# Performance work log

Hardware: AMD Instinct MI355X
Metric: run time of the kernel (lower is better)

## Reference

```python
import jax, jax.numpy as jnp
import numpy as np

N = 262144   # query points
M = 4096     # boundary points
D = 128      # d_model (m)
H = 4        # num_heads
HD = D // H  # head_dim = 32
L = 3        # num_layers
PI = float(np.pi)


def multi_feature_encoding(x):
    # x: [T, 2] -> [T, 30]; 15 fixed feature maps, hstacked
    feats = [
        x,
        x ** 2,
        (x - 1.5) ** 2,
        (x - 4.5) ** 2,
        jax.nn.sigmoid(x),
        jax.nn.sigmoid(x - 1.5),
        jax.nn.sigmoid(x - 4.5),
        x - 1.5,
        x - 4.5,
        jnp.sin(PI * x),
        jnp.cos(PI * x),
        jnp.sin(PI * x * 0.25),
        jnp.cos(PI * x * 0.25),
        jnp.sin(PI * x * 0.5),
        jnp.cos(PI * x * 0.5),
    ]
    return jnp.concatenate(feats, axis=-1)


def pos_encode(x, w, b):
    # w: [30, D], b: [D]
    return jnp.sin(multi_feature_encoding(x) @ w + b)


def setup_inputs() -> dict:
    key = jax.random.key(0)
    ks = jax.random.split(key, 24)
    s = 0.05

    def p(k, shape):
        return jax.random.normal(k, shape, dtype=jnp.float32) * s

    return {
        "query_pts": jax.random.normal(ks[0], (N, 2), dtype=jnp.float32),
        "boundary_pts": jax.random.normal(ks[1], (M, 2), dtype=jnp.float32),
        # positional encoders (query / boundary)
        "pe_w": p(ks[2], (30, D)), "pe_b": p(ks[3], (D,)),
        "bpe_w": p(ks[4], (30, D)), "bpe_b": p(ks[5], (D,)),
        # per-layer per-head q/k/v projections, stacked: [L, H, D, HD]
        "Wq": p(ks[6], (L, H, D, HD)), "bq": p(ks[7], (L, H, HD)),
        "Wk": p(ks[8], (L, H, D, HD)), "bk": p(ks[9], (L, H, HD)),
        "Wv": p(ks[10], (L, H, D, HD)), "bv": p(ks[11], (L, H, HD)),
        # attention out proj and FFN (two D->D linears) per layer
        "Wo": p(ks[12], (L, D, D)), "bo": p(ks[13], (L, D)),
        "W1": p(ks[14], (L, D, D)), "b1": p(ks[15], (L, D)),
        "W2": p(ks[16], (L, D, D)), "b2": p(ks[17], (L, D)),
        # final projector: D -> D//2 -> 3
        "pw1": p(ks[18], (D, D // 2)), "pb1": p(ks[19], (D // 2,)),
        "pw2": p(ks[20], (D // 2, 3)), "pb2": p(ks[21], (3,)),
    }


def reference(query_pts, boundary_pts, pe_w, pe_b, bpe_w, bpe_b,
              Wq, bq, Wk, bk, Wv, bv, Wo, bo, W1, b1, W2, b2,
              pw1, pb1, pw2, pb2):
    h = pos_encode(query_pts, pe_w, pe_b)[None]        # [1, N, D]
    b_enc = pos_encode(boundary_pts, bpe_w, bpe_b)[None]  # [1, M, D]

    for l in range(L):
        # batched per-head projections (equivalent to the per-head Linear loop)
        qh = jnp.einsum('btd,hde->bhte', h, Wq[l]) + bq[l][None, :, None, :]
        kh = jnp.einsum('btd,hde->bhte', b_enc, Wk[l]) + bk[l][None, :, None, :]
        vh = jnp.einsum('btd,hde->bhte', b_enc, Wv[l]) + bv[l][None, :, None, :]
        qh = qh ** 2  # squared feature map
        kh = kh ** 2
        kv_sum = jnp.einsum('bhnd,bhne->bhde', kh, vh)          # [1,H,HD,HD]
        z = 1.0 / (jnp.einsum('bhnd,bhd->bhn', qh, kh.sum(axis=2)) + 1e-6)
        attn = jnp.einsum('bhnd,bhde,bhn->bhne', qh, kv_sum, z)  # [1,H,N,HD]
        attn = attn.transpose(0, 2, 1, 3).reshape(1, -1, D)      # [1,N,D]
        attn = attn @ Wo[l] + bo[l]
        x = h + attn
        ff = jax.nn.gelu(x @ W1[l] + b1[l], approximate=False) @ W2[l] + b2[l]
        h = x + ff

    out = jax.nn.gelu(h @ pw1 + pb1, approximate=False) @ pw2 + pb2  # [1,N,3]
    return out[0]  # squeeze(0) -> [N, 3]
```

## Files before the change

kernel.cpp:

```cpp
#include <hip/hip_runtime.h>
#include <hip/hip_bf16.h>

__device__ __forceinline__ float b2f(unsigned short u) {
    return __uint_as_float(((unsigned)u) << 16);
}
__device__ __forceinline__ unsigned short f2b(float f) {
    __hip_bfloat16 h = __float2bfloat16(f);
    return *reinterpret_cast<unsigned short*>(&h);
}
__device__ __forceinline__ unsigned pk_bf16(float lo, float hi) {
    unsigned r;
    asm("v_cvt_pk_bf16_f32 %0, %1, %2" : "=v"(r) : "v"(lo), "v"(hi));
    return r;
}
__device__ __forceinline__ float exp2_hw(float x) {
    float r;
    asm("v_exp_f32 %0, %1" : "=v"(r) : "v"(x));
    return r;
}
__device__ __forceinline__ float sigm(float v) {
    return 1.f / (1.f + __expf(-v));
}
__device__ __forceinline__ float gelu_l(float x) {
    float x2 = x * x;
    float y  = x * __builtin_fmaf(0.10294535f, x2, 2.3022137f);
    float e  = exp2_hw(y);
    float r  = __builtin_amdgcn_rcpf(e + 1.f);
    return __builtin_fmaf(-x, r, x);
}

typedef __attribute__((ext_vector_type(8))) short s8v;
typedef __attribute__((ext_vector_type(4))) float f4v;
typedef __attribute__((ext_vector_type(2))) float f2v;

#define MFMA_BF16 __builtin_amdgcn_mfma_f32_16x16x32_bf16

__device__ __forceinline__ s8v mkfrag(unsigned a, unsigned b, unsigned c, unsigned d) {
    union { unsigned u[4]; s8v v; } x;
    x.u[0] = a; x.u[1] = b; x.u[2] = c; x.u[3] = d;
    return x.v;
}

__device__ __forceinline__ int fmap(int s) {
    return (s & ~31) | (((s >> 2) & 3) << 3) | (((s >> 4) & 1) << 2) | (s & 3);
}
__device__ __forceinline__ int swz_q(int q) {
    return q ^ (((q >> 7) & 7) << 3);
}

__device__ __forceinline__ void make_feats(const unsigned short* __restrict__ qpts,
                                           int r, float* __restrict__ f) {
    unsigned pq = *(const unsigned*)(qpts + (size_t)r * 2);
    float x0 = b2f((unsigned short)(pq & 0xffff));
    float x1 = b2f((unsigned short)(pq >> 16));
    const float PI = 3.14159265358979323846f;
    float a0 = x0 - 1.5f, a1 = x1 - 1.5f, c0 = x0 - 4.5f, c1 = x1 - 4.5f;
    f[0] = x0;        f[1] = x1;
    f[2] = x0 * x0;   f[3] = x1 * x1;
    f[4] = a0 * a0;   f[5] = a1 * a1;
    f[6] = c0 * c0;   f[7] = c1 * c1;
    f[8] = sigm(x0);  f[9] = sigm(x1);
    f[10] = sigm(a0); f[11] = sigm(a1);
    f[12] = sigm(c0); f[13] = sigm(c1);
    f[14] = a0;       f[15] = a1;
    f[16] = c0;       f[17] = c1;
    f[18] = __sinf(PI * x0);          f[19] = __sinf(PI * x1);
    f[20] = __cosf(PI * x0);          f[21] = __cosf(PI * x1);
    f[22] = __sinf(PI * 0.25f * x0);  f[23] = __sinf(PI * 0.25f * x1);
    f[24] = __cosf(PI * 0.25f * x0);  f[25] = __cosf(PI * 0.25f * x1);
    f[26] = __sinf(PI * 0.5f * x0);   f[27] = __sinf(PI * 0.5f * x1);
    f[28] = __cosf(PI * 0.5f * x0);   f[29] = __cosf(PI * 0.5f * x1);
}

__device__ __forceinline__ void feats8(unsigned pq, int qd, float* __restrict__ f8) {
    float x0 = b2f((unsigned short)(pq & 0xffff));
    float x1 = b2f((unsigned short)(pq >> 16));
    const float PI = 3.14159265358979323846f;
    float a0 = x0 - 1.5f, a1 = x1 - 1.5f, c0 = x0 - 4.5f, c1 = x1 - 4.5f;
    if (qd == 0) {
        f8[0] = x0;      f8[1] = x1;
        f8[2] = x0 * x0; f8[3] = x1 * x1;
        f8[4] = a0 * a0; f8[5] = a1 * a1;
        f8[6] = c0 * c0; f8[7] = c1 * c1;
    } else if (qd == 1) {
        f8[0] = sigm(x0); f8[1] = sigm(x1);
        f8[2] = sigm(a0); f8[3] = sigm(a1);
        f8[4] = sigm(c0); f8[5] = sigm(c1);
        f8[6] = a0;       f8[7] = a1;
    } else if (qd == 2) {
        f8[0] = c0; f8[1] = c1;
        f8[2] = __sinf(PI * x0);          f8[3] = __sinf(PI * x1);
        f8[4] = __cosf(PI * x0);          f8[5] = __cosf(PI * x1);
        f8[6] = __sinf(PI * 0.25f * x0);  f8[7] = __sinf(PI * 0.25f * x1);
    } else {
        f8[0] = __cosf(PI * 0.25f * x0);  f8[1] = __cosf(PI * 0.25f * x1);
        f8[2] = __sinf(PI * 0.5f * x0);   f8[3] = __sinf(PI * 0.5f * x1);
        f8[4] = __cosf(PI * 0.5f * x0);   f8[5] = __cosf(PI * 0.5f * x1);
        f8[6] = 0.f;                      f8[7] = 0.f;
    }
}

struct ConvArgs {
    const void* p[22];
    int off[23];
};

__global__ __launch_bounds__(256) void convert_kernel(
    ConvArgs a, const unsigned short* __restrict__ pe_w_raw,
    int* __restrict__ flag, unsigned short* __restrict__ canon, int total)
{
    __shared__ int cnt;
    if (threadIdx.x == 0) cnt = 0;
    __syncthreads();
    float v = b2f(pe_w_raw[threadIdx.x * 2]);
    if (!(fabsf(v) < 1.0f)) atomicAdd(&cnt, 1);
    __syncthreads();
    int isf32 = (cnt >= 16) ? 1 : 0;
    if (blockIdx.x == 0 && threadIdx.x == 0) *flag = isf32;

    int g = blockIdx.x * 256 + threadIdx.x;
    if (g >= total) return;
    int s = 0;
    #pragma unroll
    for (int i = 1; i < 23; i++) s += (g >= a.off[i]) ? 1 : 0;
    int local = g - a.off[s];
    unsigned short r;
    if (isf32) r = f2b(((const float*)a.p[s])[local]);
    else       r = ((const unsigned short*)a.p[s])[local];
    canon[g] = r;
}

__global__ __launch_bounds__(256) void encode_kernel(
    const unsigned short* __restrict__ pts,
    const unsigned short* __restrict__ w,
    const unsigned short* __restrict__ b,
    float* __restrict__ out)
{
    __shared__ __align__(16) float wsm[30 * 128];
    __shared__ float bs[128];
    int t = threadIdx.x;
    for (int i = t; i < 30 * 128; i += 256) wsm[i] = b2f(w[i]);
    if (t < 128) bs[t] = b2f(b[t]);
    __syncthreads();

    int r = blockIdx.x * 8 + (t >> 5);
    int j = t & 31;
    float f[30];
    make_feats(pts, r, f);
    float s0 = bs[j * 4 + 0], s1 = bs[j * 4 + 1], s2 = bs[j * 4 + 2], s3 = bs[j * 4 + 3];
    #pragma unroll
    for (int ff = 0; ff < 30; ff++) {
        float4 wv = *(const float4*)&wsm[ff * 128 + j * 4];
        float fv = f[ff];
        s0 += fv * wv.x; s1 += fv * wv.y; s2 += fv * wv.z; s3 += fv * wv.w;
    }
    *(float4*)&out[(size_t)r * 128 + j * 4] =
        make_float4(__sinf(s0), __sinf(s1), __sinf(s2), __sinf(s3));
}

__global__ __launch_bounds__(256) void khvh_kernel(
    const float* __restrict__ benc,
    const unsigned short* __restrict__ Wk, const unsigned short* __restrict__ bk,
    const unsigned short* __restrict__ Wv, const unsigned short* __restrict__ bv,
    float* __restrict__ kh, float* __restrict__ vh, float* __restrict__ kvz)
{
    int g = blockIdx.x * 256 + threadIdx.x;
    if (g < 12672) kvz[g] = 0.f;
    int lh = g >> 17;
    int rem = g & 131071;
    int m = rem >> 5;
    int dd = rem & 31;
    const unsigned short* wk = Wk + lh * 4096 + dd;
    const unsigned short* wv = Wv + lh * 4096 + dd;
    const float* br = benc + (size_t)m * 128;
    float ka = 0.f, va = 0.f;
    #pragma unroll 8
    for (int c = 0; c < 128; c++) {
        float bb = br[c];
        ka += bb * b2f(wk[c * 32]);
        va += bb * b2f(wv[c * 32]);
    }
    ka += b2f(bk[lh * 32 + dd]); ka = ka * ka;
    va += b2f(bv[lh * 32 + dd]);
    kh[g] = ka; vh[g] = va;
}

__global__ __launch_bounds__(1024) void kvred_kernel(
    const float* __restrict__ kh, const float* __restrict__ vh,
    float* __restrict__ kvsum, float* __restrict__ ksum)
{
    __shared__ float khs[1024];
    __shared__ float vhs[1024];
    int t = threadIdx.x;
    int lh = blockIdx.x >> 3;
    int part = blockIdx.x & 7;
    int dd = t >> 5, ee = t & 31;
    float kva = 0.f, ksa = 0.f;
    for (int ch = 0; ch < 16; ch++) {
        int base = lh * 131072 + (part * 16 + ch) * 1024;
        khs[t] = kh[base + t];
        vhs[t] = vh[base + t];
        __syncthreads();
        #pragma unroll
        for (int i = 0; i < 32; i++) {
            float kk = khs[i * 32 + dd];
            kva += kk * vhs[i * 32 + ee];
            ksa += kk;
        }
        __syncthreads();
    }
    atomicAdd(&kvsum[lh * 1024 + dd * 32 + ee], kva);
    if (ee == 0) atomicAdd(&ksum[lh * 32 + dd], ksa);
}

__global__ __launch_bounds__(256) void prep_kernel(
    const unsigned short* __restrict__ Wq, const unsigned short* __restrict__ W1,
    const unsigned short* __restrict__ W2, const unsigned short* __restrict__ pw1,
    const float* __restrict__ kvs, const float* __restrict__ kss,
    const unsigned short* __restrict__ Wo, const unsigned short* __restrict__ pe_w,
    unsigned short* __restrict__ wqT, unsigned short* __restrict__ w1T,
    unsigned short* __restrict__ w2T, unsigned short* __restrict__ pw1T,
    unsigned short* __restrict__ waT, unsigned short* __restrict__ ksT,
    unsigned short* __restrict__ pweT)
{
    int g = blockIdx.x * 256 + threadIdx.x;
    if (g < 49152) {
        int l = g >> 14, q = swz_q(g & 16383), n = q >> 7, k = q & 127;
        int na = fmap(n);
        wqT[g] = Wq[((l * 4 + (na >> 5)) * 128 + k) * 32 + (na & 31)];
    } else if (g < 98304) {
        int q0 = g - 49152; int l = q0 >> 14, q = swz_q(q0 & 16383), n = q >> 7, k = q & 127;
        w1T[q0] = W1[(l * 128 + k) * 128 + fmap(n)];
    } else if (g < 147456) {
        int q0 = g - 98304; int l = q0 >> 14, q = swz_q(q0 & 16383), n = q >> 7, k = q & 127;
        w2T[q0] = W2[(l * 128 + k) * 128 + fmap(n)];
    } else if (g < 155648) {
        int q0 = g - 147456; int q = swz_q(q0), n = q >> 7, k = q & 127;
        pw1T[q0] = pw1[k * 64 + n];
    } else if (g < 204800) {
        int q0 = g - 155648; int l = q0 >> 14, q = swz_q(q0 & 16383), n = q >> 7, k = q & 127;
        int na = fmap(n);
        int hk = k >> 5, dk = k & 31;
        const float* kvp = kvs + (l * 4 + hk) * 1024 + dk * 32;
        const unsigned short* wop = Wo + (size_t)(l * 128 + hk * 32) * 128 + na;
        float s = 0.f;
        #pragma unroll 8
        for (int j = 0; j < 32; j++) s += kvp[j] * b2f(wop[j * 128]);
        waT[q0] = f2b(s);
    } else if (g < 210944) {
        int q = g - 204800; int l = q >> 11, r = q & 2047, n = r >> 7, k = r & 127;
        unsigned short v = 0;
        if (n < 4 && (k >> 5) == n) v = f2b(kss[(l * 4 + n) * 32 + (k & 31)]);
        ksT[q] = v;
    } else if (g < 215040) {
        int q = g - 210944; int n = q >> 5, k = q & 31;
        pweT[q] = (k < 30) ? pe_w[k * 128 + fmap(n)] : (unsigned short)0;
    }
}


template<int ITERS>
__device__ __forceinline__ void stage_gll(const unsigned short* __restrict__ g,
                                          unsigned short* __restrict__ lbase,
                                          int wvi, int ln) {
    const char* gp = (const char*)g + wvi * 1024 + ln * 16;
    char* lp = (char*)lbase + wvi * 1024;
    #pragma unroll
    for (int i = 0; i < ITERS; i++) {
        __builtin_amdgcn_global_load_lds(
            (const __attribute__((address_space(1))) unsigned int*)(gp + i * 4096),
            (__attribute__((address_space(3))) unsigned int*)(lp + i * 4096),
            16, 0, 0);
    }
}

__device__ __forceinline__ s8v wfrag(const unsigned short* __restrict__ wb,
                                     int ntl, int k, int l16, int qd) {
    int lin = (ntl << 12) + (l16 << 8) + (k << 6) + (qd << 4);
    return *(const s8v*)((const char*)wb + (lin ^ ((l16 & 7) << 4)));
}

#define CAPTURE() do {                                                        \
    _Pragma("unroll")                                                         \
    for (int _s = 0; _s < 4; _s++) {                                          \
        bf0[_s] = mkfrag(pkd[0][2*_s][0], pkd[0][2*_s][1],                    \
                         pkd[0][2*_s+1][0], pkd[0][2*_s+1][1]);               \
        bf1[_s] = mkfrag(pkd[1][2*_s][0], pkd[1][2*_s][1],                    \
                         pkd[1][2*_s+1][0], pkd[1][2*_s+1][1]);               \
    }                                                                         \
} while (0)

#define MM_HALF(WB, PB, EPI...) do {                                          \
    _Pragma("unroll")                                                         \
    for (int _pp = 0; _pp < 2; _pp++) {                                       \
        const int _p = (PB) + _pp;                                            \
        f4v _x0 = {0.f,0.f,0.f,0.f}, _x1 = _x0, _y0 = _x0, _y1 = _x0;         \
        _Pragma("unroll")                                                     \
        for (int _k = 0; _k < 4; _k++) {                                      \
            s8v _wa = wfrag(WB, (_p * 2) & 3,     _k, l16, qd);               \
            s8v _wb = wfrag(WB, (_p * 2 + 1) & 3, _k, l16, qd);               \
            _x0 = MFMA_BF16(_wa, bf0[_k], _x0, 0, 0, 0);                      \
            _x1 = MFMA_BF16(_wa, bf1[_k], _x1, 0, 0, 0);                      \
            _y0 = MFMA_BF16(_wb, bf0[_k], _y0, 0, 0, 0);                      \
            _y1 = MFMA_BF16(_wb, bf1[_k], _y1, 0, 0, 0);                      \
        }                                                                     \
        { const int nt = _p * 2;     const int tile = 0; const f4v x = _x0; EPI } \
        { const int nt = _p * 2;     const int tile = 1; const f4v x = _x1; EPI } \
        { const int nt = _p * 2 + 1; const int tile = 0; const f4v x = _y0; EPI } \
        { const int nt = _p * 2 + 1; const int tile = 1; const f4v x = _y1; EPI } \
    }                                                                         \
} while (0)

#define CBDEF int cb = ((nt >> 1) << 5) + (qd << 3) + ((nt & 1) << 2)

__global__ __launch_bounds__(256) void mega_kernel(
    const unsigned short* __restrict__ qpts,
    const unsigned short* __restrict__ pweT,
    const unsigned short* __restrict__ pe_b,
    const unsigned short* __restrict__ wqT,
    const unsigned short* __restrict__ waT,
    const unsigned short* __restrict__ ksT,
    const unsigned short* __restrict__ w1T,
    const unsigned short* __restrict__ w2T,
    const unsigned short* __restrict__ bq,
    const unsigned short* __restrict__ bo,
    const unsigned short* __restrict__ b1,
    const unsigned short* __restrict__ b2,
    const unsigned short* __restrict__ pw1T,
    const unsigned short* __restrict__ pb1,
    const unsigned short* __restrict__ pw2,
    const unsigned short* __restrict__ pb2,
    void* __restrict__ outv, const int* __restrict__ flag)
{
    __shared__ __align__(16) unsigned short wbuf[2][8192];
    __shared__ __align__(16) float biasAll[12 * 128];
    __shared__ __align__(16) float pebs[128];
    __shared__ __align__(16) float pb1s[64];
    __shared__ __align__(16) float w2s4[256];
    __shared__ float pb2s[3];

    int t = threadIdx.x;
    int wvi = t >> 6, ln = t & 63, qd = ln >> 4, l16 = ln & 15;
    int row0 = blockIdx.x * 128;
    int rA0 = wvi * 32 + l16;
    unsigned short* wb0 = &wbuf[0][0];
    unsigned short* wb1 = &wbuf[1][0];

    stage_gll<4>(wqT, wb0, wvi, ln);

    for (int i = t; i < 1536; i += 256) {
        int l = i >> 9, rem = i & 511, which = rem >> 7, c = rem & 127;
        const unsigned short* bsrc = (which == 0) ? bq : (which == 1) ? bo
                                   : (which == 2) ? b1 : b2;
        biasAll[i] = b2f(bsrc[l * 128 + c]);
    }
    if (t < 128) pebs[t] = b2f(pe_b[t]);
    if (t < 64)  pb1s[t] = b2f(pb1[t]);
    if (t < 64) {
        w2s4[t * 4 + 0] = b2f(pw2[t * 3 + 0]);
        w2s4[t * 4 + 1] = b2f(pw2[t * 3 + 1]);
        w2s4[t * 4 + 2] = b2f(pw2[t * 3 + 2]);
        w2s4[t * 4 + 3] = 0.f;
    }
    if (t < 3) pb2s[t] = b2f(pb2[t]);
    __syncthreads();

    stage_gll<4>(wqT + 8192, wb1, wvi, ln);

    unsigned pkd[2][8][2];
    f2v hresv[2][8][2];

    {
        unsigned pq0 = *(const unsigned*)(qpts + (size_t)(row0 + rA0) * 2);
        unsigned pq1 = *(const unsigned*)(qpts + (size_t)(row0 + rA0 + 16) * 2);
        s8v ae0, ae1;
        {
            float f8[8]; feats8(pq0, qd, f8);
            unsigned* au = (unsigned*)&ae0;
            #pragma unroll
            for (int jj = 0; jj < 4; jj++) au[jj] = pk_bf16(f8[2 * jj], f8[2 * jj + 1]);
        }
        {
            float f8[8]; feats8(pq1, qd, f8);
            unsigned* au = (unsigned*)&ae1;
            #pragma unroll
            for (int jj = 0; jj < 4; jj++) au[jj] = pk_bf16(f8[2 * jj], f8[2 * jj + 1]);
        }
        const unsigned short* pb = pweT + l16 * 32 + qd * 8;
        #pragma unroll
        for (int nt = 0; nt < 8; nt++) {
            s8v aw = *(const s8v*)(pb + nt * 512);
            f4v x0 = {0.f, 0.f, 0.f, 0.f}, x1 = {0.f, 0.f, 0.f, 0.f};
            x0 = MFMA_BF16(aw, ae0, x0, 0, 0, 0);
            x1 = MFMA_BF16(aw, ae1, x1, 0, 0, 0);
            CBDEF;
            float4 bb = *(const float4*)&pebs[cb];
            float h0 = __sinf(x0[0] + bb.x), h1 = __sinf(x0[1] + bb.y);
            float h2 = __sinf(x0[2] + bb.z), h3 = __sinf(x0[3] + bb.w);
            f2v ha = {h0, h1}, hb = {h2, h3};
            hresv[0][nt][0] = ha; hresv[0][nt][1] = hb;
            pkd[0][nt][0] = pk_bf16(h0, h1);
            pkd[0][nt][1] = pk_bf16(h2, h3);
            float g0 = __sinf(x1[0] + bb.x), g1 = __sinf(x1[1] + bb.y);
            float g2 = __sinf(x1[2] + bb.z), g3 = __sinf(x1[3] + bb.w);
            f2v ga = {g0, g1}, gb = {g2, g3};
            hresv[1][nt][0] = ga; hresv[1][nt][1] = gb;
            pkd[1][nt][0] = pk_bf16(g0, g1);
            pkd[1][nt][1] = pk_bf16(g2, g3);
        }
    }

    s8v bf0[4], bf1[4];

    #define EPI_MM1 {                                                         \
        CBDEF;                                                                \
        float4 bb = *(const float4*)&bql[cb];                                 \
        f2v xa = {x[0], x[1]}, xb = {x[2], x[3]};                             \
        f2v ba = {bb.x, bb.y}, bc = {bb.z, bb.w};                             \
        f2v va = xa + ba, vb = xb + bc;                                       \
        f2v sa = va * va, sb = vb * vb;                                       \
        pkd[tile][nt][0] = pk_bf16(sa[0], sa[1]);                             \
        pkd[tile][nt][1] = pk_bf16(sb[0], sb[1]);                             \
    }
    #define EPI_RES(BIAS) {                                                   \
        CBDEF;                                                                \
        float4 bb = *(const float4*)&BIAS[cb];                                \
        f2v xa = {x[0], x[1]}, xb = {x[2], x[3]};                             \
        f2v ba = {bb.x, bb.y}, bc = {bb.z, bb.w};                             \
        f2v va = hresv[tile][nt][0] + xa + ba;                                \
        f2v vb = hresv[tile][nt][1] + xb + bc;                                \
        hresv[tile][nt][0] = va; hresv[tile][nt][1] = vb;                     \
        pkd[tile][nt][0] = pk_bf16(va[0], va[1]);                             \
        pkd[tile][nt][1] = pk_bf16(vb[0], vb[1]);                             \
    }
    #define EPI_GELU {                                                        \
        CBDEF;                                                                \
        float4 bb = *(const float4*)&b1l[cb];                                 \
        float g0 = gelu_l(x[0] + bb.x), g1 = gelu_l(x[1] + bb.y);             \
        float g2 = gelu_l(x[2] + bb.z), g3 = gelu_l(x[3] + bb.w);             \
        pkd[tile][nt][0] = pk_bf16(g0, g1);                                   \
        pkd[tile][nt][1] = pk_bf16(g2, g3);                                   \
    }

    for (int l = 0; l < 3; l++) {
        const float* bql = &biasAll[(l * 4 + 0) * 128];
        const float* bol = &biasAll[(l * 4 + 1) * 128];
        const float* b1l = &biasAll[(l * 4 + 2) * 128];
        const float* b2l = &biasAll[(l * 4 + 3) * 128];

        s8v kf[4];
        {
            const unsigned short* kb = ksT + l * 2048 + l16 * 128 + qd * 8;
            #pragma unroll
            for (int ks = 0; ks < 4; ks++) kf[ks] = *(const s8v*)(kb + ks * 32);
        }

        CAPTURE();
        MM_HALF(wb0, 0, EPI_MM1);
        __syncthreads();
        stage_gll<4>(waT + l * 16384, wb0, wvi, ln);
        MM_HALF(wb1, 2, EPI_MM1);
        __syncthreads();
        stage_gll<4>(waT + l * 16384 + 8192, wb1, wvi, ln);

        #pragma unroll
        for (int tile = 0; tile < 2; tile++) {
            f4v d = {0.f, 0.f, 0.f, 0.f};
            #pragma unroll
            for (int ks = 0; ks < 4; ks++) {
                s8v b = mkfrag(pkd[tile][2 * ks][0], pkd[tile][2 * ks][1],
                               pkd[tile][2 * ks + 1][0], pkd[tile][2 * ks + 1][1]);
                d = MFMA_BF16(kf[ks], b, d, 0, 0, 0);
            }
            #pragma unroll
            for (int ks = 0; ks < 4; ks++) {
                float z = 1.f / (__shfl(d[ks], l16) + 1e-6f);
                #pragma unroll
                for (int h2 = 0; h2 < 2; h2++) {
                    #pragma unroll
                    for (int j = 0; j < 2; j++) {
                        unsigned w = pkd[tile][2 * ks + h2][j];
                        float lo = __uint_as_float(w << 16) * z;
                        float hi = __uint_as_float(w & 0xffff0000u) * z;
                        pkd[tile][2 * ks + h2][j] = pk_bf16(lo, hi);
                    }
                }
            }
        }

        CAPTURE();
        MM_HALF(wb0, 0, EPI_RES(bol));
        __syncthreads();
        stage_gll<4>(w1T + l * 16384, wb0, wvi, ln);
        MM_HALF(wb1, 2, EPI_RES(bol));
        __syncthreads();
        stage_gll<4>(w1T + l * 16384 + 8192, wb1, wvi, ln);

        CAPTURE();
        MM_HALF(wb0, 0, EPI_GELU);
        __syncthreads();
        stage_gll<4>(w2T + l * 16384, wb0, wvi, ln);
        MM_HALF(wb1, 2, EPI_GELU);
        __syncthreads();
        stage_gll<4>(w2T + l * 16384 + 8192, wb1, wvi, ln);

        CAPTURE();
        MM_HALF(wb0, 0, EPI_RES(b2l));
        __syncthreads();
        if (l < 2) stage_gll<4>(wqT + (l + 1) * 16384, wb0, wvi, ln);
        else       stage_gll<4>(pw1T, wb0, wvi, ln);
        MM_HALF(wb1, 2, EPI_RES(b2l));
        __syncthreads();
        if (l < 2) stage_gll<4>(wqT + (l + 1) * 16384 + 8192, wb1, wvi, ln);
    }

    {
        CAPTURE();
        float pt0[3] = {0.f, 0.f, 0.f}, pt1[3] = {0.f, 0.f, 0.f};
        #pragma unroll
        for (int p = 0; p < 2; p++) {
            f4v y00 = {0.f,0.f,0.f,0.f}, y01 = y00, y10 = y00, y11 = y00;
            #pragma unroll
            for (int ks = 0; ks < 4; ks++) {
                s8v wa = wfrag(wb0, p * 2,     ks, l16, qd);
                s8v wb = wfrag(wb0, p * 2 + 1, ks, l16, qd);
                y00 = MFMA_BF16(wa, bf0[ks], y00, 0, 0, 0);
                y01 = MFMA_BF16(wa, bf1[ks], y01, 0, 0, 0);
                y10 = MFMA_BF16(wb, bf0[ks], y10, 0, 0, 0);
                y11 = MFMA_BF16(wb, bf1[ks], y11, 0, 0, 0);
            }
            #pragma unroll
            for (int e = 0; e < 2; e++) {
                int c0 = (p * 2 + e) * 16 + qd * 4;
                float4 bb = *(const float4*)&pb1s[c0];
                f4v ya = e ? y10 : y00;
                f4v yb = e ? y11 : y01;
                #pragma unroll
                for (int i = 0; i < 4; i++) {
                    float bbi = (i == 0) ? bb.x : (i == 1) ? bb.y : (i == 2) ? bb.z : bb.w;
                    float4 w = *(const float4*)&w2s4[(c0 + i) * 4];
                    float ga = gelu_l(ya[i] + bbi);
                    float gb = gelu_l(yb[i] + bbi);
                    pt0[0] = fmaf(ga, w.x, pt0[0]);
                    pt0[1] = fmaf(ga, w.y, pt0[1]);
                    pt0[2] = fmaf(ga, w.z, pt0[2]);
                    pt1[0] = fmaf(gb, w.x, pt1[0]);
                    pt1[1] = fmaf(gb, w.y, pt1[1]);
                    pt1[2] = fmaf(gb, w.z, pt1[2]);
                }
            }
        }
        #pragma unroll
        for (int c = 0; c < 3; c++) {
            pt0[c] += __shfl_xor(pt0[c], 16); pt0[c] += __shfl_xor(pt0[c], 32);
            pt1[c] += __shfl_xor(pt1[c], 16); pt1[c] += __shfl_xor(pt1[c], 32);
            pt0[c] += pb2s[c]; pt1[c] += pb2s[c];
        }
        if (ln < 16) {
            size_t r0 = (size_t)(row0 + rA0) * 3;
            size_t r1 = (size_t)(row0 + rA0 + 16) * 3;
            if (*flag) {
                float* o = (float*)outv;
                o[r0] = pt0[0]; o[r0 + 1] = pt0[1]; o[r0 + 2] = pt0[2];
                o[r1] = pt1[0]; o[r1 + 1] = pt1[1]; o[r1 + 2] = pt1[2];
            } else {
                unsigned short* o = (unsigned short*)outv;
                o[r0] = f2b(pt0[0]); o[r0 + 1] = f2b(pt0[1]); o[r0 + 2] = f2b(pt0[2]);
                o[r1] = f2b(pt1[0]); o[r1 + 1] = f2b(pt1[1]); o[r1 + 2] = f2b(pt1[2]);
            }
        }
    }
}

extern "C" void kernel_launch(void* const* d_in, const int* in_sizes, int n_in,
                              void* d_out, int out_size, void* d_ws, size_t ws_size,
                              hipStream_t stream) {
    const int N = in_sizes[0] / 2;
    const int M = in_sizes[1] / 2;

    ConvArgs ca;
    int total = 0;
    for (int i = 0; i < 22; i++) { ca.p[i] = d_in[i]; ca.off[i] = total; total += in_sizes[i]; }
    ca.off[22] = total;

    float* ws = (float*)d_ws;
    int* flag = (int*)ws;
    unsigned short* canon = (unsigned short*)(ws + 16);
    size_t canonF = ((size_t)(total + 1) / 2 + 15) & ~(size_t)15;
    float* b_enc = ws + 16 + canonF;
    float* khb   = b_enc + (size_t)M * 128;
    float* vhb   = khb + (size_t)12 * M * 32;
    float* kvs   = vhb + (size_t)12 * M * 32;
    float* kss   = kvs + 12288;
    unsigned short* wqT  = (unsigned short*)(kss + 384);
    unsigned short* waT  = wqT + 49152;
    unsigned short* w1T  = waT + 49152;
    unsigned short* w2T  = w1T + 49152;
    unsigned short* ksT  = w2T + 49152;
    unsigned short* pw1T = ksT + 6144;
    unsigned short* pweT = pw1T + 8192;

    const unsigned short* c_qpts = canon + ca.off[0];
    const unsigned short* c_bpts = canon + ca.off[1];
    const unsigned short* c_pew  = canon + ca.off[2];
    const unsigned short* c_peb  = canon + ca.off[3];
    const unsigned short* c_bpew = canon + ca.off[4];
    const unsigned short* c_bpeb = canon + ca.off[5];
    const unsigned short* c_Wq   = canon + ca.off[6];
    const unsigned short* c_bq   = canon + ca.off[7];
    const unsigned short* c_Wk   = canon + ca.off[8];
    const unsigned short* c_bk   = canon + ca.off[9];
    const unsigned short* c_Wv   = canon + ca.off[10];
    const unsigned short* c_bv   = canon + ca.off[11];
    const unsigned short* c_Wo   = canon + ca.off[12];
    const unsigned short* c_bo   = canon + ca.off[13];
    const unsigned short* c_W1   = canon + ca.off[14];
    const unsigned short* c_b1   = canon + ca.off[15];
    const unsigned short* c_W2   = canon + ca.off[16];
    const unsigned short* c_b2   = canon + ca.off[17];
    const unsigned short* c_pw1  = canon + ca.off[18];
    const unsigned short* c_pb1  = canon + ca.off[19];
    const unsigned short* c_pw2  = canon + ca.off[20];
    const unsigned short* c_pb2  = canon + ca.off[21];

    convert_kernel<<<(total + 255) / 256, 256, 0, stream>>>(
        ca, (const unsigned short*)d_in[2], flag, canon, total);

    encode_kernel<<<M / 8, 256, 0, stream>>>(c_bpts, c_bpew, c_bpeb, b_enc);
    khvh_kernel<<<(12 * M * 32) / 256, 256, 0, stream>>>(
        b_enc, c_Wk, c_bk, c_Wv, c_bv, khb, vhb, kvs);
    kvred_kernel<<<96, 1024, 0, stream>>>(khb, vhb, kvs, kss);
    prep_kernel<<<215040 / 256, 256, 0, stream>>>(
        c_Wq, c_W1, c_W2, c_pw1, kvs, kss, c_Wo, c_pew,
        wqT, w1T, w2T, pw1T, waT, ksT, pweT);

    mega_kernel<<<N / 128, 256, 0, stream>>>(
        c_qpts, pweT, c_peb, wqT, waT, ksT, w1T, w2T,
        c_bq, c_bo, c_b1, c_b2, pw1T, c_pb1, c_pw2, c_pb2, d_out, flag);
}
```

Baseline: 357.4 us.

## Drop input canonicalization pass and fuse K/V projection into reduction kernel

Removes the convert kernel that copied every input (including the large query point array) into a bf16 canonical buffer. Each kernel now detects the input dtype itself with a wave ballot and reads raw f32 or bf16 directly. The kh/vh projection kernel is merged into the KV reduction kernel, which computes projections in-block straight into shared memory, so the intermediate global kh/vh buffers and one launch are gone. In exchange, every kernel carries duplicated dtype branches, and the merged kernel recomputes the projections with more blocks, each relying on atomics.

```diff
diff --git a/kernel.cpp b/kernel.cpp
--- a/kernel.cpp
+++ b/kernel.cpp
@@ -41,6 +41,18 @@
     return x.v;
 }
 
+__device__ __forceinline__ int detect_f32(const unsigned short* __restrict__ raw) {
+    int ln = threadIdx.x & 63;
+    int c = 0;
+    #pragma unroll
+    for (int j = 0; j < 4; j++) {
+        float v = b2f(raw[(ln * 4 + j) * 2]);
+        unsigned long long m = __ballot(!(fabsf(v) < 1.0f));
+        c += __popcll(m);
+    }
+    return c >= 16;
+}
+
 __device__ __forceinline__ int fmap(int s) {
     return (s & ~31) | (((s >> 2) & 3) << 3) | (((s >> 4) & 1) << 2) | (s & 3);
 }
@@ -48,11 +60,7 @@
     return q ^ (((q >> 7) & 7) << 3);
 }
 
-__device__ __forceinline__ void make_feats(const unsigned short* __restrict__ qpts,
-                                           int r, float* __restrict__ f) {
-    unsigned pq = *(const unsigned*)(qpts + (size_t)r * 2);
-    float x0 = b2f((unsigned short)(pq & 0xffff));
-    float x1 = b2f((unsigned short)(pq >> 16));
+__device__ __forceinline__ void make_feats2(float x0, float x1, float* __restrict__ f) {
     const float PI = 3.14159265358979323846f;
     float a0 = x0 - 1.5f, a1 = x1 - 1.5f, c0 = x0 - 4.5f, c1 = x1 - 4.5f;
     f[0] = x0;        f[1] = x1;
@@ -72,9 +80,7 @@
     f[28] = __cosf(PI * 0.5f * x0);   f[29] = __cosf(PI * 0.5f * x1);
 }
 
-__device__ __forceinline__ void feats8(unsigned pq, int qd, float* __restrict__ f8) {
-    float x0 = b2f((unsigned short)(pq & 0xffff));
-    float x1 = b2f((unsigned short)(pq >> 16));
+__device__ __forceinline__ void feats8(float x0, float x1, int qd, float* __restrict__ f8) {
     const float PI = 3.14159265358979323846f;
     float a0 = x0 - 1.5f, a1 = x1 - 1.5f, c0 = x0 - 4.5f, c1 = x1 - 4.5f;
     if (qd == 0) {
@@ -100,53 +106,56 @@
     }
 }
 
-struct ConvArgs {
-    const void* p[22];
-    int off[23];
-};
-
-__global__ __launch_bounds__(256) void convert_kernel(
-    ConvArgs a, const unsigned short* __restrict__ pe_w_raw,
-    int* __restrict__ flag, unsigned short* __restrict__ canon, int total)
+__device__ __forceinline__ float ldr(const unsigned short* __restrict__ p, int idx, int isf32) {
+    float v;
+    if (isf32) v = ((const float*)p)[idx];
+    else       v = b2f(p[idx]);
+    return v;
+}
+__device__ __forceinline__ unsigned short ldb(const unsigned short* __restrict__ p, int idx, int isf32) {
+    unsigned short v;
+    if (isf32) v = f2b(((const float*)p)[idx]);
+    else       v = p[idx];
+    return v;
+}
+
+__global__ __launch_bounds__(256) void encode_kernel(
+    const unsigned short* __restrict__ pts_raw,
+    const unsigned short* __restrict__ w_raw,
+    const unsigned short* __restrict__ b_raw,
+    const unsigned short* __restrict__ pe_w_raw,
+    float* __restrict__ out, float* __restrict__ kvz)
 {
-    __shared__ int cnt;
-    if (threadIdx.x == 0) cnt = 0;
-    __syncthreads();
-    float v = b2f(pe_w_raw[threadIdx.x * 2]);
-    if (!(fabsf(v) < 1.0f)) atomicAdd(&cnt, 1);
-    __syncthreads();
-    int isf32 = (cnt >= 16) ? 1 : 0;
-    if (blockIdx.x == 0 && threadIdx.x == 0) *flag = isf32;
-
-    int g = blockIdx.x * 256 + threadIdx.x;
-    if (g >= total) return;
-    int s = 0;
-    #pragma unroll
-    for (int i = 1; i < 23; i++) s += (g >= a.off[i]) ? 1 : 0;
-    int local = g - a.off[s];
-    unsigned short r;
-    if (isf32) r = f2b(((const float*)a.p[s])[local]);
-    else       r = ((const unsigned short*)a.p[s])[local];
-    canon[g] = r;
-}
-
-__global__ __launch_bounds__(256) void encode_kernel(
-    const unsigned short* __restrict__ pts,
-    const unsigned short* __restrict__ w,
-    const unsigned short* __restrict__ b,
-    float* __restrict__ out)
-{
+    int isf32 = detect_f32(pe_w_raw);
     __shared__ __align__(16) float wsm[30 * 128];
     __shared__ float bs[128];
     int t = threadIdx.x;
-    for (int i = t; i < 30 * 128; i += 256) wsm[i] = b2f(w[i]);
-    if (t < 128) bs[t] = b2f(b[t]);
+    int g = blockIdx.x * 256 + t;
+    if (g < 12672) kvz[g] = 0.f;
+
+    if (isf32) {
+        const float* w = (const float*)w_raw;
+        for (int i = t; i < 30 * 128; i += 256) wsm[i] = w[i];
+        if (t < 128) bs[t] = ((const float*)b_raw)[t];
+    } else {
+        for (int i = t; i < 30 * 128; i += 256) wsm[i] = b2f(w_raw[i]);
+        if (t < 128) bs[t] = b2f(b_raw[t]);
+    }
     __syncthreads();
 
     int r = blockIdx.x * 8 + (t >> 5);
     int j = t & 31;
+    float x0, x1;
+    if (isf32) {
+        float2 p = ((const float2*)pts_raw)[r];
+        x0 = p.x; x1 = p.y;
+    } else {
+        unsigned pq = ((const unsigned*)pts_raw)[r];
+        x0 = b2f((unsigned short)(pq & 0xffff));
+        x1 = b2f((unsigned short)(pq >> 16));
+    }
     float f[30];
-    make_feats(pts, r, f);
+    make_feats2(x0, x1, f);
     float s0 = bs[j * 4 + 0], s1 = bs[j * 4 + 1], s2 = bs[j * 4 + 2], s3 = bs[j * 4 + 3];
     #pragma unroll
     for (int ff = 0; ff < 30; ff++) {
@@ -158,59 +167,66 @@
         make_float4(__sinf(s0), __sinf(s1), __sinf(s2), __sinf(s3));
 }
 
-__global__ __launch_bounds__(256) void khvh_kernel(
+__global__ __launch_bounds__(1024) void khvred_kernel(
     const float* __restrict__ benc,
-    const unsigned short* __restrict__ Wk, const unsigned short* __restrict__ bk,
-    const unsigned short* __restrict__ Wv, const unsigned short* __restrict__ bv,
-    float* __restrict__ kh, float* __restrict__ vh, float* __restrict__ kvz)
-{
-    int g = blockIdx.x * 256 + threadIdx.x;
-    if (g < 12672) kvz[g] = 0.f;
-    int lh = g >> 17;
-    int rem = g & 131071;
-    int m = rem >> 5;
-    int dd = rem & 31;
-    const unsigned short* wk = Wk + lh * 4096 + dd;
-    const unsigned short* wv = Wv + lh * 4096 + dd;
-    const float* br = benc + (size_t)m * 128;
-    float ka = 0.f, va = 0.f;
-    #pragma unroll 8
-    for (int c = 0; c < 128; c++) {
-        float bb = br[c];
-        ka += bb * b2f(wk[c * 32]);
-        va += bb * b2f(wv[c * 32]);
-    }
-    ka += b2f(bk[lh * 32 + dd]); ka = ka * ka;
-    va += b2f(bv[lh * 32 + dd]);
-    kh[g] = ka; vh[g] = va;
-}
-
-__global__ __launch_bounds__(1024) void kvred_kernel(
-    const float* __restrict__ kh, const float* __restrict__ vh,
+    const unsigned short* __restrict__ Wk_raw, const unsigned short* __restrict__ bk_raw,
+    const unsigned short* __restrict__ Wv_raw, const unsigned short* __restrict__ bv_raw,
+    const unsigned short* __restrict__ pe_w_raw,
     float* __restrict__ kvsum, float* __restrict__ ksum)
 {
+    int isf32 = detect_f32(pe_w_raw);
     __shared__ float khs[1024];
     __shared__ float vhs[1024];
     int t = threadIdx.x;
-    int lh = blockIdx.x >> 3;
-    int part = blockIdx.x & 7;
-    int dd = t >> 5, ee = t & 31;
+    int lh = blockIdx.x >> 5;
+    int part = blockIdx.x & 31;
+    int mm = t >> 5, dd = t & 31;
+    int dd2 = t >> 5, ee = t & 31;
     float kva = 0.f, ksa = 0.f;
-    for (int ch = 0; ch < 16; ch++) {
-        int base = lh * 131072 + (part * 16 + ch) * 1024;
-        khs[t] = kh[base + t];
-        vhs[t] = vh[base + t];
+
+    for (int ch = 0; ch < 4; ch++) {
+        int m = part * 128 + ch * 32 + mm;
+        const float* br = benc + (size_t)m * 128;
+        float ka, va;
+        if (isf32) {
+            const float* wk = (const float*)Wk_raw + lh * 4096 + dd;
+            const float* wv = (const float*)Wv_raw + lh * 4096 + dd;
+            float a = 0.f, b = 0.f;
+            #pragma unroll 8
+            for (int c = 0; c < 128; c++) {
+                float bb = br[c];
+                a += bb * wk[c * 32];
+                b += bb * wv[c * 32];
+            }
+            ka = a + ((const float*)bk_raw)[lh * 32 + dd];
+            va = b + ((const float*)bv_raw)[lh * 32 + dd];
+        } else {
+            const unsigned short* wk = Wk_raw + lh * 4096 + dd;
+            const unsigned short* wv = Wv_raw + lh * 4096 + dd;
+            float a = 0.f, b = 0.f;
+            #pragma unroll 8
+            for (int c = 0; c < 128; c++) {
+                float bb = br[c];
+                a += bb * b2f(wk[c * 32]);
+                b += bb * b2f(wv[c * 32]);
+            }
+            ka = a + b2f(bk_raw[lh * 32 + dd]);
+            va = b + b2f(bv_raw[lh * 32 + dd]);
+        }
+        ka = ka * ka;
+        khs[mm * 32 + dd] = ka;
+        vhs[mm * 32 + dd] = va;
         __syncthreads();
         #pragma unroll
         for (int i = 0; i < 32; i++) {
-            float kk = khs[i * 32 + dd];
+            float kk = khs[i * 32 + dd2];
             kva += kk * vhs[i * 32 + ee];
             ksa += kk;
         }
         __syncthreads();
     }
-    atomicAdd(&kvsum[lh * 1024 + dd * 32 + ee], kva);
-    if (ee == 0) atomicAdd(&ksum[lh * 32 + dd], ksa);
+    atomicAdd(&kvsum[lh * 1024 + dd2 * 32 + ee], kva);
+    if (ee == 0) atomicAdd(&ksum[lh * 32 + dd2], ksa);
 }
 
 __global__ __launch_bounds__(256) void prep_kernel(
@@ -223,29 +239,36 @@
     unsigned short* __restrict__ waT, unsigned short* __restrict__ ksT,
     unsigned short* __restrict__ pweT)
 {
+    int isf32 = detect_f32(pe_w);
     int g = blockIdx.x * 256 + threadIdx.x;
     if (g < 49152) {
         int l = g >> 14, q = swz_q(g & 16383), n = q >> 7, k = q & 127;
         int na = fmap(n);
-        wqT[g] = Wq[((l * 4 + (na >> 5)) * 128 + k) * 32 + (na & 31)];
+        wqT[g] = ldb(Wq, ((l * 4 + (na >> 5)) * 128 + k) * 32 + (na & 31), isf32);
     } else if (g < 98304) {
         int q0 = g - 49152; int l = q0 >> 14, q = swz_q(q0 & 16383), n = q >> 7, k = q & 127;
-        w1T[q0] = W1[(l * 128 + k) * 128 + fmap(n)];
+        w1T[q0] = ldb(W1, (l * 128 + k) * 128 + fmap(n), isf32);
     } else if (g < 147456) {
         int q0 = g - 98304; int l = q0 >> 14, q = swz_q(q0 & 16383), n = q >> 7, k = q & 127;
-        w2T[q0] = W2[(l * 128 + k) * 128 + fmap(n)];
+        w2T[q0] = ldb(W2, (l * 128 + k) * 128 + fmap(n), isf32);
     } else if (g < 155648) {
         int q0 = g - 147456; int q = swz_q(q0), n = q >> 7, k = q & 127;
-        pw1T[q0] = pw1[k * 64 + n];
+        pw1T[q0] = ldb(pw1, k * 64 + n, isf32);
     } else if (g < 204800) {
         int q0 = g - 155648; int l = q0 >> 14, q = swz_q(q0 & 16383), n = q >> 7, k = q & 127;
         int na = fmap(n);
         int hk = k >> 5, dk = k & 31;
         const float* kvp = kvs + (l * 4 + hk) * 1024 + dk * 32;
-        const unsigned short* wop = Wo + (size_t)(l * 128 + hk * 32) * 128 + na;
         float s = 0.f;
-        #pragma unroll 8
-        for (int j = 0; j < 32; j++) s += kvp[j] * b2f(wop[j * 128]);
+        if (isf32) {
+            const float* wop = (const float*)Wo + (size_t)(l * 128 + hk * 32) * 128 + na;
+            #pragma unroll 8
+            for (int j = 0; j < 32; j++) s += kvp[j] * wop[j * 128];
+        } else {
+            const unsigned short* wop = Wo + (size_t)(l * 128 + hk * 32) * 128 + na;
+            #pragma unroll 8
+            for (int j = 0; j < 32; j++) s += kvp[j] * b2f(wop[j * 128]);
+        }
         waT[q0] = f2b(s);
     } else if (g < 210944) {
         int q = g - 204800; int l = q >> 11, r = q & 2047, n = r >> 7, k = r & 127;
@@ -254,7 +277,7 @@
         ksT[q] = v;
     } else if (g < 215040) {
         int q = g - 210944; int n = q >> 5, k = q & 31;
-        pweT[q] = (k < 30) ? pe_w[k * 128 + fmap(n)] : (unsigned short)0;
+        pweT[q] = (k < 30) ? ldb(pe_w, k * 128 + fmap(n), isf32) : (unsigned short)0;
     }
 }
 
@@ -330,7 +353,8 @@
     const unsigned short* __restrict__ pb1,
     const unsigned short* __restrict__ pw2,
     const unsigned short* __restrict__ pb2,
-    void* __restrict__ outv, const int* __restrict__ flag)
+    const unsigned short* __restrict__ pe_w_raw,
+    void* __restrict__ outv)
 {
     __shared__ __align__(16) unsigned short wbuf[2][8192];
     __shared__ __align__(16) float biasAll[12 * 128];
@@ -339,6 +363,7 @@
     __shared__ __align__(16) float w2s4[256];
     __shared__ float pb2s[3];
 
+    int isf32 = detect_f32(pe_w_raw);
     int t = threadIdx.x;
     int wvi = t >> 6, ln = t & 63, qd = ln >> 4, l16 = ln & 15;
     int row0 = blockIdx.x * 128;
@@ -348,21 +373,40 @@
 
     stage_gll<4>(wqT, wb0, wvi, ln);
 
-    for (int i = t; i < 1536; i += 256) {
-        int l = i >> 9, rem = i & 511, which = rem >> 7, c = rem & 127;
-        const unsigned short* bsrc = (which == 0) ? bq : (which == 1) ? bo
-                                   : (which == 2) ? b1 : b2;
-        biasAll[i] = b2f(bsrc[l * 128 + c]);
-    }
-    if (t < 128) pebs[t] = b2f(pe_b[t]);
-    if (t < 64)  pb1s[t] = b2f(pb1[t]);
-    if (t < 64) {
-        w2s4[t * 4 + 0] = b2f(pw2[t * 3 + 0]);
-        w2s4[t * 4 + 1] = b2f(pw2[t * 3 + 1]);
-        w2s4[t * 4 + 2] = b2f(pw2[t * 3 + 2]);
-        w2s4[t * 4 + 3] = 0.f;
-    }
-    if (t < 3) pb2s[t] = b2f(pb2[t]);
+    if (isf32) {
+        for (int i = t; i < 1536; i += 256) {
+            int l = i >> 9, rem = i & 511, which = rem >> 7, c = rem & 127;
+            const unsigned short* bsrc = (which == 0) ? bq : (which == 1) ? bo
+                                       : (which == 2) ? b1 : b2;
+            biasAll[i] = ((const float*)bsrc)[l * 128 + c];
+        }
+        if (t < 128) pebs[t] = ((const float*)pe_b)[t];
+        if (t < 64)  pb1s[t] = ((const float*)pb1)[t];
+        if (t < 64) {
+            const float* w = (const float*)pw2;
+            w2s4[t * 4 + 0] = w[t * 3 + 0];
+            w2s4[t * 4 + 1] = w[t * 3 + 1];
+            w2s4[t * 4 + 2] = w[t * 3 + 2];
+            w2s4[t * 4 + 3] = 0.f;
+        }
+        if (t < 3) pb2s[t] = ((const float*)pb2)[t];
+    } else {
+        for (int i = t; i < 1536; i += 256) {
+            int l = i >> 9, rem = i & 511, which = rem >> 7, c = rem & 127;
+            const unsigned short* bsrc = (which == 0) ? bq : (which == 1) ? bo
+                                       : (which == 2) ? b1 : b2;
+            biasAll[i] = b2f(bsrc[l * 128 + c]);
+        }
+        if (t < 128) pebs[t] = b2f(pe_b[t]);
+        if (t < 64)  pb1s[t] = b2f(pb1[t]);
+        if (t < 64) {
+            w2s4[t * 4 + 0] = b2f(pw2[t * 3 + 0]);
+            w2s4[t * 4 + 1] = b2f(pw2[t * 3 + 1]);
+            w2s4[t * 4 + 2] = b2f(pw2[t * 3 + 2]);
+            w2s4[t * 4 + 3] = 0.f;
+        }
+        if (t < 3) pb2s[t] = b2f(pb2[t]);
+    }
     __syncthreads();
 
     stage_gll<4>(wqT + 8192, wb1, wvi, ln);
@@ -371,17 +415,28 @@
     f2v hresv[2][8][2];
 
     {
-        unsigned pq0 = *(const unsigned*)(qpts + (size_t)(row0 + rA0) * 2);
-        unsigned pq1 = *(const unsigned*)(qpts + (size_t)(row0 + rA0 + 16) * 2);
+        float x0a, x1a, x0b, x1b;
+        if (isf32) {
+            float2 p0 = ((const float2*)qpts)[row0 + rA0];
+            float2 p1 = ((const float2*)qpts)[row0 + rA0 + 16];
+            x0a = p0.x; x1a = p0.y; x0b = p1.x; x1b = p1.y;
+        } else {
+            unsigned pq0 = ((const unsigned*)qpts)[row0 + rA0];
+            unsigned pq1 = ((const unsigned*)qpts)[row0 + rA0 + 16];
+            x0a = b2f((unsigned short)(pq0 & 0xffff));
+            x1a = b2f((unsigned short)(pq0 >> 16));
+            x0b = b2f((unsigned short)(pq1 & 0xffff));
+            x1b = b2f((unsigned short)(pq1 >> 16));
+        }
         s8v ae0, ae1;
         {
-            float f8[8]; feats8(pq0, qd, f8);
+            float f8[8]; feats8(x0a, x1a, qd, f8);
             unsigned* au = (unsigned*)&ae0;
             #pragma unroll
             for (int jj = 0; jj < 4; jj++) au[jj] = pk_bf16(f8[2 * jj], f8[2 * jj + 1]);
         }
         {
-            float f8[8]; feats8(pq1, qd, f8);
+            float f8[8]; feats8(x0b, x1b, qd, f8);
             unsigned* au = (unsigned*)&ae1;
             #pragma unroll
             for (int jj = 0; jj < 4; jj++) au[jj] = pk_bf16(f8[2 * jj], f8[2 * jj + 1]);
@@ -559,7 +614,7 @@
         if (ln < 16) {
             size_t r0 = (size_t)(row0 + rA0) * 3;
             size_t r1 = (size_t)(row0 + rA0 + 16) * 3;
-            if (*flag) {
+            if (isf32) {
                 float* o = (float*)outv;
                 o[r0] = pt0[0]; o[r0 + 1] = pt0[1]; o[r0 + 2] = pt0[2];
                 o[r1] = pt1[0]; o[r1 + 1] = pt1[1]; o[r1 + 2] = pt1[2];
@@ -578,19 +633,32 @@
     const int N = in_sizes[0] / 2;
     const int M = in_sizes[1] / 2;
 
-    ConvArgs ca;
-    int total = 0;
-    for (int i = 0; i < 22; i++) { ca.p[i] = d_in[i]; ca.off[i] = total; total += in_sizes[i]; }
-    ca.off[22] = total;
+    const unsigned short* r_qpts = (const unsigned short*)d_in[0];
+    const unsigned short* r_bpts = (const unsigned short*)d_in[1];
+    const unsigned short* r_pew  = (const unsigned short*)d_in[2];
+    const unsigned short* r_peb  = (const unsigned short*)d_in[3];
+    const unsigned short* r_bpew = (const unsigned short*)d_in[4];
+    const unsigned short* r_bpeb = (const unsigned short*)d_in[5];
+    const unsigned short* r_Wq   = (const unsigned short*)d_in[6];
+    const unsigned short* r_bq   = (const unsigned short*)d_in[7];
+    const unsigned short* r_Wk   = (const unsigned short*)d_in[8];
+    const unsigned short* r_bk   = (const unsigned short*)d_in[9];
+    const unsigned short* r_Wv   = (const unsigned short*)d_in[10];
+    const unsigned short* r_bv   = (const unsigned short*)d_in[11];
+    const unsigned short* r_Wo   = (const unsigned short*)d_in[12];
+    const unsigned short* r_bo   = (const unsigned short*)d_in[13];
+    const unsigned short* r_W1   = (const unsigned short*)d_in[14];
+    const unsigned short* r_b1   = (const unsigned short*)d_in[15];
+    const unsigned short* r_W2   = (const unsigned short*)d_in[16];
+    const unsigned short* r_b2   = (const unsigned short*)d_in[17];
+    const unsigned short* r_pw1  = (const unsigned short*)d_in[18];
+    const unsigned short* r_pb1  = (const unsigned short*)d_in[19];
+    const unsigned short* r_pw2  = (const unsigned short*)d_in[20];
+    const unsigned short* r_pb2  = (const unsigned short*)d_in[21];
 
     float* ws = (float*)d_ws;
-    int* flag = (int*)ws;
-    unsigned short* canon = (unsigned short*)(ws + 16);
-    size_t canonF = ((size_t)(total + 1) / 2 + 15) & ~(size_t)15;
-    float* b_enc = ws + 16 + canonF;
-    float* khb   = b_enc + (size_t)M * 128;
-    float* vhb   = khb + (size_t)12 * M * 32;
-    float* kvs   = vhb + (size_t)12 * M * 32;
+    float* b_enc = ws;
+    float* kvs   = b_enc + (size_t)M * 128;
     float* kss   = kvs + 12288;
     unsigned short* wqT  = (unsigned short*)(kss + 384);
     unsigned short* waT  = wqT + 49152;
@@ -600,41 +668,14 @@
     unsigned short* pw1T = ksT + 6144;
     unsigned short* pweT = pw1T + 8192;
 
-    const unsigned short* c_qpts = canon + ca.off[0];
-    const unsigned short* c_bpts = canon + ca.off[1];
-    const unsigned short* c_pew  = canon + ca.off[2];
-    const unsigned short* c_peb  = canon + ca.off[3];
-    const unsigned short* c_bpew = canon + ca.off[4];
-    const unsigned short* c_bpeb = canon + ca.off[5];
-    const unsigned short* c_Wq   = canon + ca.off[6];
-    const unsigned short* c_bq   = canon + ca.off[7];
-    const unsigned short* c_Wk   = canon + ca.off[8];
-    const unsigned short* c_bk   = canon + ca.off[9];
-    const unsigned short* c_Wv   = canon + ca.off[10];
-    const unsigned short* c_bv   = canon + ca.off[11];
-    const unsigned short* c_Wo   = canon + ca.off[12];
-    const unsigned short* c_bo   = canon + ca.off[13];
-    const unsigned short* c_W1   = canon + ca.off[14];
-    const unsigned short* c_b1   = canon + ca.off[15];
-    const unsigned short* c_W2   = canon + ca.off[16];
-    const unsigned short* c_b2   = canon + ca.off[17];
-    const unsigned short* c_pw1  = canon + ca.off[18];
-    const unsigned short* c_pb1  = canon + ca.off[19];
-    const unsigned short* c_pw2  = canon + ca.off[20];
-    const unsigned short* c_pb2  = canon + ca.off[21];
-
-    convert_kernel<<<(total + 255) / 256, 256, 0, stream>>>(
-        ca, (const unsigned short*)d_in[2], flag, canon, total);
-
-    encode_kernel<<<M / 8, 256, 0, stream>>>(c_bpts, c_bpew, c_bpeb, b_enc);
-    khvh_kernel<<<(12 * M * 32) / 256, 256, 0, stream>>>(
-        b_enc, c_Wk, c_bk, c_Wv, c_bv, khb, vhb, kvs);
-    kvred_kernel<<<96, 1024, 0, stream>>>(khb, vhb, kvs, kss);
+    encode_kernel<<<M / 8, 256, 0, stream>>>(
+        r_bpts, r_bpew, r_bpeb, r_pew, b_enc, kvs);
+    khvred_kernel<<<384, 1024, 0, stream>>>(
+        b_enc, r_Wk, r_bk, r_Wv, r_bv, r_pew, kvs, kss);
     prep_kernel<<<215040 / 256, 256, 0, stream>>>(
-        c_Wq, c_W1, c_W2, c_pw1, kvs, kss, c_Wo, c_pew,
+        r_Wq, r_W1, r_W2, r_pw1, kvs, kss, r_Wo, r_pew,
         wqT, w1T, w2T, pw1T, waT, ksT, pweT);
-
     mega_kernel<<<N / 128, 256, 0, stream>>>(
-        c_qpts, pweT, c_peb, wqT, waT, ksT, w1T, w2T,
-        c_bq, c_bo, c_b1, c_b2, pw1T, c_pb1, c_pw2, c_pb2, d_out, flag);
-}
+        r_qpts, pweT, r_peb, wqT, waT, ksT, w1T, w2T,
+        r_bq, r_bo, r_b1, r_b2, pw1T, r_pb1, r_pw2, r_pb2, r_pew, d_out);
+}
```

After: 356.9 us. No clear change (-0.1%).
